# Performance work log

Hardware: AMD Instinct MI355X
Metric: run time of the kernel (lower is better)

The kernel has to match this reference:

```python
import jax, jax.numpy as jnp
import numpy as np

TEMP1, TEMP2, TEMP3 = 4.0, 5.0, 10.0  # forward() default temps
EPS = 1e-8


def setup_inputs() -> dict:
    key = jax.random.key(0)
    k1, k2 = jax.random.split(key)
    B, L, D = 64, 64, 512
    return {
        "ecg_embs": jax.random.normal(k1, (B, L, D), dtype=jnp.float32),
        "sent_embs": jax.random.normal(k2, (B, L, D), dtype=jnp.float32),
    }


def reference(ecg_embs, sent_embs):
    # Fully-batched version of the original per-sample Python loop.
    # i indexes the sentence (query) sample, j the ecg (context) sample.
    B, L, D = ecg_embs.shape
    # scores[i,j,s,q] = <ecg[j,s,:], sent[i,q,:]>  == contextT @ query in torch
    scores = jnp.einsum('jsd,iqd->ijsq', ecg_embs, sent_embs)
    # 1st softmax over query axis q
    attn = jax.nn.softmax(scores, axis=-1)
    # transpose to (i,j,q,s), temperature-scale, 2nd softmax over source axis s
    attn = jax.nn.softmax(TEMP1 * jnp.swapaxes(attn, -1, -2), axis=-1)  # (i,j,q,s)
    # weightedContext[i,j,q,:] = sum_s attn[i,j,q,s] * ecg[j,s,:]
    wctx = jnp.einsum('ijqs,jsd->ijqd', attn, ecg_embs)
    sent = sent_embs[:, None]  # (i,1,q,d) broadcast over j
    w12 = jnp.sum(sent * wctx, axis=-1)
    w1 = jnp.linalg.norm(sent, axis=-1)
    w2 = jnp.linalg.norm(wctx, axis=-1)
    cos = w12 / jnp.maximum(w1 * w2, EPS)  # (i,j,q)
    # row_sim.mul_(temp2).exp_().sum(dim=1).log() ; similarities[j,i] (cat along dim=1)
    sim = TEMP3 * jnp.log(jnp.sum(jnp.exp(TEMP2 * cos), axis=-1)).T  # (j,i)
    labels = jnp.arange(B)
    logp0 = jax.nn.log_softmax(sim, axis=-1)
    logp1 = jax.nn.log_softmax(sim.T, axis=-1)
    loss0 = -jnp.mean(logp0[labels, labels])
    loss1 = -jnp.mean(logp1[labels, labels])
    # att_maps: list of attn[i] from iteration i == diagonal (i==j) attention,
    # each shaped (1, queryL, ih=1, iw=sourceL); stacked -> (B, 1, L, 1, L)
    att_maps = attn[labels, labels][:, None, :, None, :]
    return (loss0 + loss1) / 2.0, att_maps
```

## Files before the change

kernel.cpp:

```cpp
#include <hip/hip_runtime.h>
#include <math.h>

typedef __attribute__((ext_vector_type(8))) short short8;
typedef __attribute__((ext_vector_type(4))) float f32x4;
typedef unsigned int uint;
typedef unsigned short ushort;

#define T1 4.0f
#define T2 5.0f
#define T3 10.0f
#define EPSF 1e-8f
#define SST 68

__device__ inline ushort f2bf(float x) {
    union { float f; uint u; } a; a.f = x;
    uint r = a.u + 0x7FFFu + ((a.u >> 16) & 1u);
    return (ushort)(r >> 16);
}
__device__ inline float bf2f(ushort h) {
    union { uint u; float f; } a; a.u = ((uint)h) << 16;
    return a.f;
}

#define GLDS(gsrc, ldst) \
    __builtin_amdgcn_global_load_lds( \
        (const __attribute__((address_space(1))) uint*)(gsrc), \
        (__attribute__((address_space(3))) uint*)(ldst), 16, 0, 0)

__global__ __launch_bounds__(256) void prep_kernel(
        const float* __restrict__ ecg, const float* __restrict__ sent,
        char* __restrict__ EH, char* __restrict__ EL,
        char* __restrict__ SH, char* __restrict__ SL, float* __restrict__ w1) {
    __shared__ float partial[256];
    const int bid = blockIdx.x;
    const int tensor = bid >> 6, idx = bid & 63;
    const float* src = (tensor ? sent : ecg) + (size_t)idx * 32768;
    char* dh = (tensor ? SH : EH) + (size_t)idx * 65536;
    char* dl = (tensor ? SL : EL) + (size_t)idx * 65536;
    const int tid = threadIdx.x;
    const int r = tid & 63;
    float s2 = 0.f;
    #pragma unroll
    for (int it = 0; it < 4; it++) {
        int kc = it * 4 + (tid >> 6);
        const float* p = src + r * 512 + kc * 32;
        char* oh = dh + kc * 4096 + r * 64;
        char* ol = dl + kc * 4096 + r * 64;
        #pragma unroll
        for (int c = 0; c < 4; c++) {
            float4 v0 = *(const float4*)(p + c * 8);
            float4 v1 = *(const float4*)(p + c * 8 + 4);
            float x[8] = {v0.x, v0.y, v0.z, v0.w, v1.x, v1.y, v1.z, v1.w};
            uint hw[4], lw[4];
            #pragma unroll
            for (int e = 0; e < 4; e++) {
                float a0 = x[2 * e], a1 = x[2 * e + 1];
                ushort h0 = f2bf(a0), h1 = f2bf(a1);
                hw[e] = (uint)h0 | ((uint)h1 << 16);
                ushort l0 = f2bf(a0 - bf2f(h0)), l1 = f2bf(a1 - bf2f(h1));
                lw[e] = (uint)l0 | ((uint)l1 << 16);
                s2 += a0 * a0 + a1 * a1;
            }
            int phys = (c + (r >> 1)) & 3;
            uint4 H; H.x = hw[0]; H.y = hw[1]; H.z = hw[2]; H.w = hw[3];
            *(uint4*)(oh + phys * 16) = H;
            uint4 L; L.x = lw[0]; L.y = lw[1]; L.z = lw[2]; L.w = lw[3];
            *(uint4*)(ol + phys * 16) = L;
        }
    }
    partial[tid] = s2;
    __syncthreads();
    if (tensor == 1 && tid < 64) {
        float t = partial[tid] + partial[tid + 64] + partial[tid + 128] + partial[tid + 192];
        w1[idx * 64 + tid] = sqrtf(t);
    }
}

__global__ __launch_bounds__(256) void gprep_kernel(
        const char* __restrict__ EH, const char* __restrict__ EL, char* __restrict__ Gp) {
    __shared__ __align__(16) char lds[8192];
    const int j = blockIdx.x;
    const int tid = threadIdx.x;
    const int wv = tid >> 6, lane = tid & 63;
    const int wq = wv >> 1, wn = wv & 1;
    const int quad = lane >> 4, ln = lane & 15;
    const char* srcH = EH + (size_t)j * 65536 + wv * 1024 + lane * 16;
    const char* srcL = EL + (size_t)j * 65536 + wv * 1024 + lane * 16;

    int ao[2], bo[2];
    #pragma unroll
    for (int mi = 0; mi < 2; mi++) {
        int R = 32 * wq + 16 * mi + ln;
        ao[mi] = R * 64 + ((quad + (R >> 1)) & 3) * 16;
    }
    #pragma unroll
    for (int ni = 0; ni < 2; ni++) {
        int R = 32 * wn + 16 * ni + ln;
        bo[ni] = R * 64 + ((quad + (R >> 1)) & 3) * 16;
    }

    f32x4 acc[2][2];
    #pragma unroll
    for (int a = 0; a < 2; a++)
        #pragma unroll
        for (int b = 0; b < 2; b++) acc[a][b] = (f32x4){0.f, 0.f, 0.f, 0.f};

    for (int kc = 0; kc < 16; kc++) {
        GLDS(srcH + (size_t)kc * 4096, lds + wv * 1024);
        GLDS(srcL + (size_t)kc * 4096, lds + 4096 + wv * 1024);
        __syncthreads();
        short8 ah[2], al[2], bh[2], bl[2];
        #pragma unroll
        for (int mi = 0; mi < 2; mi++) {
            ah[mi] = *(const short8*)(lds + ao[mi]);
            al[mi] = *(const short8*)(lds + 4096 + ao[mi]);
        }
        #pragma unroll
        for (int ni = 0; ni < 2; ni++) {
            bh[ni] = *(const short8*)(lds + bo[ni]);
            bl[ni] = *(const short8*)(lds + 4096 + bo[ni]);
        }
        #pragma unroll
        for (int mi = 0; mi < 2; mi++)
            #pragma unroll
            for (int ni = 0; ni < 2; ni++) {
                acc[mi][ni] = __builtin_amdgcn_mfma_f32_16x16x32_bf16(ah[mi], bh[ni], acc[mi][ni], 0, 0, 0);
                acc[mi][ni] = __builtin_amdgcn_mfma_f32_16x16x32_bf16(ah[mi], bl[ni], acc[mi][ni], 0, 0, 0);
                acc[mi][ni] = __builtin_amdgcn_mfma_f32_16x16x32_bf16(al[mi], bh[ni], acc[mi][ni], 0, 0, 0);
            }
        __syncthreads();
    }
    #pragma unroll
    for (int mi = 0; mi < 2; mi++)
        #pragma unroll
        for (int ni = 0; ni < 2; ni++)
            #pragma unroll
            for (int r = 0; r < 4; r++) {
                int t = 32 * wq + 16 * mi + quad * 4 + r;
                int u = 32 * wn + 16 * ni + ln;
                float g = acc[mi][ni][r];
                ushort h = f2bf(g);
                ushort l = f2bf(g - bf2f(h));
                char* base = Gp + (size_t)j * 16384 + t * 128 + (((u >> 3) + t) & 7) * 16 + (u & 7) * 2;
                *(ushort*)base = h;
                *(ushort*)(base + 8192) = l;
            }
}

__global__ __launch_bounds__(256, 4) void pair_kernel(
        const char* __restrict__ EH, const char* __restrict__ EL,
        const char* __restrict__ SH, const char* __restrict__ SL,
        const char* __restrict__ Gp, const float* __restrict__ w1g,
        float* __restrict__ simval, float* __restrict__ out) {

    __shared__ __align__(16) char lds[33792];
    __shared__ __align__(16) float mz[64];
    __shared__ float w12all[256], w2all[256];

    const int tid = threadIdx.x;
    const int bn = blockIdx.x;
    const int xcd = bn & 7, slot = bn >> 3;
    const int T = xcd * 8 + (slot >> 4);
    const int wp = slot & 15;
    const int bi = (T >> 3) * 4 + (wp >> 2);
    const int bj = (T & 7) * 4 + (wp & 3);
    const int i0 = bi * 2, j0 = bj * 2;

    const int wv = tid >> 6, lane = tid & 63;
    const int wq = wv >> 1, wn = wv & 1;
    const int quad = lane >> 4, ln = lane & 15;

    int aoff[4], boff[4];
    #pragma unroll
    for (int mi = 0; mi < 4; mi++) {
        int R = 64 * (mi >> 1) + 32 * wq + 16 * (mi & 1) + ln;
        aoff[mi] = R * 64 + ((quad + (R >> 1)) & 3) * 16;
    }
    #pragma unroll
    for (int ni = 0; ni < 4; ni++) {
        int R = 64 * (ni >> 1) + 32 * wn + 16 * (ni & 1) + ln;
        boff[ni] = 16384 + R * 64 + ((quad + (R >> 1)) & 3) * 16;
    }

    const char* gA; const char* gB; int ldoff;
    if (wv == 0)      { gA = EH + (size_t)j0 * 65536;       gB = EH + (size_t)(j0 + 1) * 65536; ldoff = 0; }
    else if (wv == 1) { gA = EL + (size_t)j0 * 65536;       gB = EL + (size_t)(j0 + 1) * 65536; ldoff = 8192; }
    else if (wv == 2) { gA = SH + (size_t)i0 * 65536;       gB = SH + (size_t)(i0 + 1) * 65536; ldoff = 16384; }
    else              { gA = SL + (size_t)i0 * 65536;       gB = SL + (size_t)(i0 + 1) * 65536; ldoff = 24576; }
    gA += lane * 16; gB += lane * 16;

    f32x4 acc[4][4];
    #pragma unroll
    for (int a = 0; a < 4; a++)
        #pragma unroll
        for (int b = 0; b < 4; b++) acc[a][b] = (f32x4){0.f, 0.f, 0.f, 0.f};

    for (int kc = 0; kc < 16; kc++) {
        #pragma unroll
        for (int n = 0; n < 4; n++) GLDS(gA + n * 1024, lds + ldoff + n * 1024);
        #pragma unroll
        for (int n = 0; n < 4; n++) GLDS(gB + n * 1024, lds + ldoff + 4096 + n * 1024);
        gA += 4096; gB += 4096;
        __syncthreads();
        short8 bh[4], bl[4];
        #pragma unroll
        for (int ni = 0; ni < 4; ni++) {
            bh[ni] = *(const short8*)(lds + boff[ni]);
            bl[ni] = *(const short8*)(lds + boff[ni] + 8192);
        }
        #pragma unroll
        for (int mi = 0; mi < 4; mi++) {
            short8 ah = *(const short8*)(lds + aoff[mi]);
            short8 al = *(const short8*)(lds + aoff[mi] + 8192);
            #pragma unroll
            for (int ni = 0; ni < 4; ni++) {
                acc[mi][ni] = __builtin_amdgcn_mfma_f32_16x16x32_bf16(ah, bh[ni], acc[mi][ni], 0, 0, 0);
                acc[mi][ni] = __builtin_amdgcn_mfma_f32_16x16x32_bf16(ah, bl[ni], acc[mi][ni], 0, 0, 0);
                acc[mi][ni] = __builtin_amdgcn_mfma_f32_16x16x32_bf16(al, bh[ni], acc[mi][ni], 0, 0, 0);
            }
        }
        __syncthreads();
    }

    float* SsT = (float*)lds;
    float* yT  = (float*)lds;
    char*  Pb  = lds + 17408;

    #pragma unroll
    for (int pr = 0; pr < 4; pr++) {
        const int a = pr >> 1, b = pr & 1;
        const int i = i0 + b, j = j0 + a;

        #pragma unroll
        for (int dm = 0; dm < 2; dm++)
            #pragma unroll
            for (int dn = 0; dn < 2; dn++) {
                int s0 = 32 * wq + 16 * dm + quad * 4;
                int q  = 32 * wn + 16 * dn + ln;
                *(f32x4*)(SsT + q * SST + s0) = acc[2 * a + dm][2 * b + dn];
            }
        __syncthreads();

        {
            const int s = tid >> 2, c = tid & 3;
            float vv[16]; float m = -1e30f;
            #pragma unroll
            for (int t = 0; t < 16; t++) {
                int tt = (t + 4 * c) & 15;
                vv[t] = SsT[(16 * c + tt) * SST + s];
                m = fmaxf(m, vv[t]);
            }
            m = fmaxf(m, __shfl_xor(m, 1));
            m = fmaxf(m, __shfl_xor(m, 2));
            float sum = 0.f;
            #pragma unroll
            for (int t = 0; t < 16; t++) sum += __expf(vv[t] - m);
            sum += __shfl_xor(sum, 1);
            sum += __shfl_xor(sum, 2);
            if (c == 0) mz[s] = m + __logf(sum);
        }
        __syncthreads();

        {
            const int q = tid >> 2, c = tid & 3;
            float sc[16], at[16];
            #pragma unroll
            for (int r4 = 0; r4 < 4; r4++)
                *(f32x4*)(sc + 4 * r4) = *(const f32x4*)(SsT + q * SST + 16 * c + 4 * r4);
            float mzv[16];
            #pragma unroll
            for (int r4 = 0; r4 < 4; r4++)
                *(f32x4*)(mzv + 4 * r4) = *(const f32x4*)(mz + 16 * c + 4 * r4);
            float m2 = -1e30f;
            #pragma unroll
            for (int t = 0; t < 16; t++) {
                at[t] = __expf(sc[t] - mzv[t]);
                m2 = fmaxf(m2, T1 * at[t]);
            }
            m2 = fmaxf(m2, __shfl_xor(m2, 1));
            m2 = fmaxf(m2, __shfl_xor(m2, 2));
            float sum = 0.f;
            #pragma unroll
            for (int t = 0; t < 16; t++) { at[t] = __expf(T1 * at[t] - m2); sum += at[t]; }
            sum += __shfl_xor(sum, 1);
            sum += __shfl_xor(sum, 2);
            float inv = 1.f / sum;
            float p12 = 0.f;
            #pragma unroll
            for (int t = 0; t < 16; t++) { at[t] *= inv; p12 += at[t] * sc[t]; }
            p12 += __shfl_xor(p12, 1);
            p12 += __shfl_xor(p12, 2);
            if (c == 0) w12all[pr * 64 + q] = p12;

            if (i == j) {
                float* om = out + 1 + (size_t)i * 4096;
                #pragma unroll
                for (int t = 0; t < 16; t++) om[q * 64 + c * 16 + t] = at[t];
            }

            uint hw[8], lw[8];
            #pragma unroll
            for (int e = 0; e < 8; e++) {
                ushort h0 = f2bf(at[2 * e]), h1 = f2bf(at[2 * e + 1]);
                hw[e] = (uint)h0 | ((uint)h1 << 16);
                ushort l0 = f2bf(at[2 * e] - bf2f(h0)), l1 = f2bf(at[2 * e + 1] - bf2f(h1));
                lw[e] = (uint)l0 | ((uint)l1 << 16);
            }
            int p0 = (2 * c + q) & 7, p1 = (2 * c + 1 + q) & 7;
            uint4 W;
            W.x = hw[0]; W.y = hw[1]; W.z = hw[2]; W.w = hw[3];
            *(uint4*)(Pb + q * 128 + p0 * 16) = W;
            W.x = hw[4]; W.y = hw[5]; W.z = hw[6]; W.w = hw[7];
            *(uint4*)(Pb + q * 128 + p1 * 16) = W;
            W.x = lw[0]; W.y = lw[1]; W.z = lw[2]; W.w = lw[3];
            *(uint4*)(Pb + 8192 + q * 128 + p0 * 16) = W;
            W.x = lw[4]; W.y = lw[5]; W.z = lw[6]; W.w = lw[7];
            *(uint4*)(Pb + 8192 + q * 128 + p1 * 16) = W;
        }
        __syncthreads();

        {
            const char* gs = Gp + (size_t)j * 16384 + wv * 4096 + lane * 16;
            char* gd = lds + wv * 4096;
            GLDS(gs,        gd);
            GLDS(gs + 1024, gd + 1024);
            GLDS(gs + 2048, gd + 2048);
            GLDS(gs + 3072, gd + 3072);
        }
        __syncthreads();

        f32x4 acc2[2][2];
        #pragma unroll
        for (int x = 0; x < 2; x++)
            #pragma unroll
            for (int y = 0; y < 2; y++) acc2[x][y] = (f32x4){0.f, 0.f, 0.f, 0.f};
        #pragma unroll
        for (int ch = 0; ch < 2; ch++) {
            short8 pah[2], pal[2], gbh[2], gbl[2];
            #pragma unroll
            for (int m2i = 0; m2i < 2; m2i++) {
                int q = 32 * wq + 16 * m2i + ln;
                int ph = ((ch * 4 + quad) + q) & 7;
                pah[m2i] = *(const short8*)(Pb + q * 128 + ph * 16);
                pal[m2i] = *(const short8*)(Pb + 8192 + q * 128 + ph * 16);
            }
            #pragma unroll
            for (int n2i = 0; n2i < 2; n2i++) {
                int u = 32 * wn + 16 * n2i + ln;
                int ph = ((ch * 4 + quad) + u) & 7;
                gbh[n2i] = *(const short8*)(lds + u * 128 + ph * 16);
                gbl[n2i] = *(const short8*)(lds + 8192 + u * 128 + ph * 16);
            }
            #pragma unroll
            for (int m2i = 0; m2i < 2; m2i++)
                #pragma unroll
                for (int n2i = 0; n2i < 2; n2i++) {
                    acc2[m2i][n2i] = __builtin_amdgcn_mfma_f32_16x16x32_bf16(pah[m2i], gbh[n2i], acc2[m2i][n2i], 0, 0, 0);
                    acc2[m2i][n2i] = __builtin_amdgcn_mfma_f32_16x16x32_bf16(pah[m2i], gbl[n2i], acc2[m2i][n2i], 0, 0, 0);
                    acc2[m2i][n2i] = __builtin_amdgcn_mfma_f32_16x16x32_bf16(pal[m2i], gbh[n2i], acc2[m2i][n2i], 0, 0, 0);
                }
        }
        __syncthreads();

        #pragma unroll
        for (int m2i = 0; m2i < 2; m2i++)
            #pragma unroll
            for (int n2i = 0; n2i < 2; n2i++) {
                int q0 = 32 * wq + 16 * m2i + quad * 4;
                int t  = 32 * wn + 16 * n2i + ln;
                *(f32x4*)(yT + t * SST + q0) = acc2[m2i][n2i];
            }
        __syncthreads();

        {
            const int q = tid >> 2, c = tid & 3;
            int p0 = (2 * c + q) & 7, p1 = (2 * c + 1 + q) & 7;
            uint4 H0 = *(const uint4*)(Pb + q * 128 + p0 * 16);
            uint4 H1 = *(const uint4*)(Pb + q * 128 + p1 * 16);
            uint4 L0 = *(const uint4*)(Pb + 8192 + q * 128 + p0 * 16);
            uint4 L1 = *(const uint4*)(Pb + 8192 + q * 128 + p1 * 16);
            uint hw[8] = {H0.x,H0.y,H0.z,H0.w, H1.x,H1.y,H1.z,H1.w};
            uint lw[8] = {L0.x,L0.y,L0.z,L0.w, L1.x,L1.y,L1.z,L1.w};
            float s = 0.f;
            #pragma unroll
            for (int e = 0; e < 8; e++) {
                float q0v = bf2f((ushort)(hw[e] & 0xFFFFu)) + bf2f((ushort)(lw[e] & 0xFFFFu));
                float q1v = bf2f((ushort)(hw[e] >> 16))     + bf2f((ushort)(lw[e] >> 16));
                s += q0v * yT[(16 * c + 2 * e) * SST + q];
                s += q1v * yT[(16 * c + 2 * e + 1) * SST + q];
            }
            s += __shfl_xor(s, 1);
            s += __shfl_xor(s, 2);
            if (c == 0) w2all[pr * 64 + q] = s;
        }
        __syncthreads();
    }

    {
        const int pr = wv;
        const int ii = i0 + (pr & 1), jj = j0 + (pr >> 1);
        float w2 = sqrtf(fmaxf(w2all[pr * 64 + lane], 0.f));
        float cosv = w12all[pr * 64 + lane] / fmaxf(w1g[ii * 64 + lane] * w2, EPSF);
        float e = __expf(T2 * cosv);
        #pragma unroll
        for (int off = 32; off; off >>= 1) e += __shfl_down(e, off);
        if (lane == 0) simval[ii * 64 + jj] = T3 * __logf(e);
    }
}

__global__ __launch_bounds__(256) void loss_kernel(const float* __restrict__ val,
                                                   float* __restrict__ out) {
    __shared__ float v[4096];
    const int tid = threadIdx.x;
    #pragma unroll
    for (int k = 0; k < 4; k++)
        ((float4*)v)[tid + k * 256] = ((const float4*)val)[tid + k * 256];
    __syncthreads();
    if (tid < 64) {
        int i = tid;
        float rmax = -1e30f, cmax = -1e30f;
        for (int jj = 0; jj < 64; jj++) {
            rmax = fmaxf(rmax, v[i * 64 + jj]);
            cmax = fmaxf(cmax, v[jj * 64 + i]);
        }
        float rs = 0.f, cs = 0.f;
        for (int jj = 0; jj < 64; jj++) {
            rs += __expf(v[i * 64 + jj] - rmax);
            cs += __expf(v[jj * 64 + i] - cmax);
        }
        float rlse = rmax + __logf(rs);
        float clse = cmax + __logf(cs);
        float part = 2.f * v[i * 64 + i] - rlse - clse;
        #pragma unroll
        for (int off = 32; off; off >>= 1) part += __shfl_down(part, off);
        if (i == 0) out[0] = -part / 128.f;
    }
}

extern "C" void kernel_launch(void* const* d_in, const int* in_sizes, int n_in,
                              void* d_out, int out_size, void* d_ws, size_t ws_size,
                              hipStream_t stream) {
    (void)in_sizes; (void)n_in; (void)out_size; (void)ws_size;
    const float* ecg  = (const float*)d_in[0];
    const float* sent = (const float*)d_in[1];
    float* out = (float*)d_out;

    char* ws = (char*)d_ws;
    float* w1v  = (float*)ws;
    float* simv = (float*)(ws + 16384);
    char* EH = ws + 32768;
    char* EL = EH + (size_t)64 * 65536;
    char* SH = EL + (size_t)64 * 65536;
    char* SL = SH + (size_t)64 * 65536;
    char* Gp = SL + (size_t)64 * 65536;

    prep_kernel <<<128, 256, 0, stream>>>(ecg, sent, EH, EL, SH, SL, w1v);
    gprep_kernel<<<64,  256, 0, stream>>>(EH, EL, Gp);
    pair_kernel <<<1024, 256, 0, stream>>>(EH, EL, SH, SL, Gp, w1v, simv, out);
    loss_kernel <<<1,   256, 0, stream>>>(simv, out);
}
```

Baseline: 150.4 us.

## Double-buffer pair kernel K loop, split gprep into more blocks, parallelize loss reductions

The pair kernel's K-loop now double-buffers LDS (64KB). It prefetches the next chunk while computing the current one, using vmcnt waits and raw barriers, and lowers the launch-bound occupancy hint from 4 to 2. gprep is split into 4x more blocks, each computing one 16-row tile with direct global loads and no LDS staging. The loss kernel computes row and column log-sum-exps on separate wavefronts. The aim is to hide global load latency and add parallelism, at the cost of fewer resident blocks per CU in the pair kernel.

```diff
diff --git a/kernel.cpp b/kernel.cpp
--- a/kernel.cpp
+++ b/kernel.cpp
@@ -78,82 +78,52 @@
 
 __global__ __launch_bounds__(256) void gprep_kernel(
         const char* __restrict__ EH, const char* __restrict__ EL, char* __restrict__ Gp) {
-    __shared__ __align__(16) char lds[8192];
-    const int j = blockIdx.x;
+    const int b = blockIdx.x;
+    const int j = b >> 2, tq = b & 3;
     const int tid = threadIdx.x;
     const int wv = tid >> 6, lane = tid & 63;
-    const int wq = wv >> 1, wn = wv & 1;
     const int quad = lane >> 4, ln = lane & 15;
-    const char* srcH = EH + (size_t)j * 65536 + wv * 1024 + lane * 16;
-    const char* srcL = EL + (size_t)j * 65536 + wv * 1024 + lane * 16;
-
-    int ao[2], bo[2];
-    #pragma unroll
-    for (int mi = 0; mi < 2; mi++) {
-        int R = 32 * wq + 16 * mi + ln;
-        ao[mi] = R * 64 + ((quad + (R >> 1)) & 3) * 16;
-    }
-    #pragma unroll
-    for (int ni = 0; ni < 2; ni++) {
-        int R = 32 * wn + 16 * ni + ln;
-        bo[ni] = R * 64 + ((quad + (R >> 1)) & 3) * 16;
-    }
-
-    f32x4 acc[2][2];
-    #pragma unroll
-    for (int a = 0; a < 2; a++)
-        #pragma unroll
-        for (int b = 0; b < 2; b++) acc[a][b] = (f32x4){0.f, 0.f, 0.f, 0.f};
-
+    const char* srcH = EH + (size_t)j * 65536;
+    const char* srcL = EL + (size_t)j * 65536;
+
+    const int Ra = 16 * tq + ln;
+    const int ao = Ra * 64 + ((quad + (Ra >> 1)) & 3) * 16;
+    const int Rb = 16 * wv + ln;
+    const int bo = Rb * 64 + ((quad + (Rb >> 1)) & 3) * 16;
+
+    f32x4 acc = (f32x4){0.f, 0.f, 0.f, 0.f};
+    #pragma unroll 4
     for (int kc = 0; kc < 16; kc++) {
-        GLDS(srcH + (size_t)kc * 4096, lds + wv * 1024);
-        GLDS(srcL + (size_t)kc * 4096, lds + 4096 + wv * 1024);
-        __syncthreads();
-        short8 ah[2], al[2], bh[2], bl[2];
-        #pragma unroll
-        for (int mi = 0; mi < 2; mi++) {
-            ah[mi] = *(const short8*)(lds + ao[mi]);
-            al[mi] = *(const short8*)(lds + 4096 + ao[mi]);
-        }
-        #pragma unroll
-        for (int ni = 0; ni < 2; ni++) {
-            bh[ni] = *(const short8*)(lds + bo[ni]);
-            bl[ni] = *(const short8*)(lds + 4096 + bo[ni]);
-        }
-        #pragma unroll
-        for (int mi = 0; mi < 2; mi++)
-            #pragma unroll
-            for (int ni = 0; ni < 2; ni++) {
-                acc[mi][ni] = __builtin_amdgcn_mfma_f32_16x16x32_bf16(ah[mi], bh[ni], acc[mi][ni], 0, 0, 0);
-                acc[mi][ni] = __builtin_amdgcn_mfma_f32_16x16x32_bf16(ah[mi], bl[ni], acc[mi][ni], 0, 0, 0);
-                acc[mi][ni] = __builtin_amdgcn_mfma_f32_16x16x32_bf16(al[mi], bh[ni], acc[mi][ni], 0, 0, 0);
-            }
-        __syncthreads();
-    }
-    #pragma unroll
-    for (int mi = 0; mi < 2; mi++)
-        #pragma unroll
-        for (int ni = 0; ni < 2; ni++)
-            #pragma unroll
-            for (int r = 0; r < 4; r++) {
-                int t = 32 * wq + 16 * mi + quad * 4 + r;
-                int u = 32 * wn + 16 * ni + ln;
-                float g = acc[mi][ni][r];
-                ushort h = f2bf(g);
-                ushort l = f2bf(g - bf2f(h));
-                char* base = Gp + (size_t)j * 16384 + t * 128 + (((u >> 3) + t) & 7) * 16 + (u & 7) * 2;
-                *(ushort*)base = h;
-                *(ushort*)(base + 8192) = l;
-            }
-}
-
-__global__ __launch_bounds__(256, 4) void pair_kernel(
+        const char* ph = srcH + (size_t)kc * 4096;
+        const char* pl = srcL + (size_t)kc * 4096;
+        short8 ah = *(const short8*)(ph + ao);
+        short8 al = *(const short8*)(pl + ao);
+        short8 bh = *(const short8*)(ph + bo);
+        short8 bl = *(const short8*)(pl + bo);
+        acc = __builtin_amdgcn_mfma_f32_16x16x32_bf16(ah, bh, acc, 0, 0, 0);
+        acc = __builtin_amdgcn_mfma_f32_16x16x32_bf16(ah, bl, acc, 0, 0, 0);
+        acc = __builtin_amdgcn_mfma_f32_16x16x32_bf16(al, bh, acc, 0, 0, 0);
+    }
+    #pragma unroll
+    for (int rr = 0; rr < 4; rr++) {
+        int t = 16 * tq + quad * 4 + rr;
+        int u = 16 * wv + ln;
+        float g = acc[rr];
+        ushort h = f2bf(g);
+        ushort l = f2bf(g - bf2f(h));
+        char* base = Gp + (size_t)j * 16384 + t * 128 + (((u >> 3) + t) & 7) * 16 + (u & 7) * 2;
+        *(ushort*)base = h;
+        *(ushort*)(base + 8192) = l;
+    }
+}
+
+__global__ __launch_bounds__(256, 2) void pair_kernel(
         const char* __restrict__ EH, const char* __restrict__ EL,
         const char* __restrict__ SH, const char* __restrict__ SL,
         const char* __restrict__ Gp, const float* __restrict__ w1g,
         float* __restrict__ simval, float* __restrict__ out) {
 
-    __shared__ __align__(16) char lds[33792];
+    __shared__ __align__(16) char lds[65536];
     __shared__ __align__(16) float mz[64];
     __shared__ float w12all[256], w2all[256];
 
@@ -195,23 +165,17 @@
         #pragma unroll
         for (int b = 0; b < 4; b++) acc[a][b] = (f32x4){0.f, 0.f, 0.f, 0.f};
 
-    for (int kc = 0; kc < 16; kc++) {
-        #pragma unroll
-        for (int n = 0; n < 4; n++) GLDS(gA + n * 1024, lds + ldoff + n * 1024);
-        #pragma unroll
-        for (int n = 0; n < 4; n++) GLDS(gB + n * 1024, lds + ldoff + 4096 + n * 1024);
-        gA += 4096; gB += 4096;
-        __syncthreads();
+    auto compute = [&](const char* L) {
         short8 bh[4], bl[4];
         #pragma unroll
         for (int ni = 0; ni < 4; ni++) {
-            bh[ni] = *(const short8*)(lds + boff[ni]);
-            bl[ni] = *(const short8*)(lds + boff[ni] + 8192);
+            bh[ni] = *(const short8*)(L + boff[ni]);
+            bl[ni] = *(const short8*)(L + boff[ni] + 8192);
         }
         #pragma unroll
         for (int mi = 0; mi < 4; mi++) {
-            short8 ah = *(const short8*)(lds + aoff[mi]);
-            short8 al = *(const short8*)(lds + aoff[mi] + 8192);
+            short8 ah = *(const short8*)(L + aoff[mi]);
+            short8 al = *(const short8*)(L + aoff[mi] + 8192);
             #pragma unroll
             for (int ni = 0; ni < 4; ni++) {
                 acc[mi][ni] = __builtin_amdgcn_mfma_f32_16x16x32_bf16(ah, bh[ni], acc[mi][ni], 0, 0, 0);
@@ -219,8 +183,35 @@
                 acc[mi][ni] = __builtin_amdgcn_mfma_f32_16x16x32_bf16(al, bh[ni], acc[mi][ni], 0, 0, 0);
             }
         }
-        __syncthreads();
-    }
+    };
+
+    #pragma unroll
+    for (int n = 0; n < 4; n++) GLDS(gA + n * 1024, lds + ldoff + n * 1024);
+    #pragma unroll
+    for (int n = 0; n < 4; n++) GLDS(gB + n * 1024, lds + ldoff + 4096 + n * 1024);
+
+    for (int kc = 0; kc < 15; kc++) {
+        {
+            const char* pA = gA + (size_t)(kc + 1) * 4096;
+            const char* pB = gB + (size_t)(kc + 1) * 4096;
+            char* db = lds + ((kc + 1) & 1) * 32768 + ldoff;
+            #pragma unroll
+            for (int n = 0; n < 4; n++) GLDS(pA + n * 1024, db + n * 1024);
+            #pragma unroll
+            for (int n = 0; n < 4; n++) GLDS(pB + n * 1024, db + 4096 + n * 1024);
+        }
+        asm volatile("s_waitcnt vmcnt(8)" ::: "memory");
+        __builtin_amdgcn_s_barrier();
+        asm volatile("" ::: "memory");
+        compute(lds + (kc & 1) * 32768);
+        asm volatile("" ::: "memory");
+        __builtin_amdgcn_s_barrier();
+    }
+    asm volatile("s_waitcnt vmcnt(0)" ::: "memory");
+    __builtin_amdgcn_s_barrier();
+    asm volatile("" ::: "memory");
+    compute(lds + 32768);
+    __syncthreads();
 
     float* SsT = (float*)lds;
     float* yT  = (float*)lds;
@@ -411,6 +402,7 @@
 __global__ __launch_bounds__(256) void loss_kernel(const float* __restrict__ val,
                                                    float* __restrict__ out) {
     __shared__ float v[4096];
+    __shared__ float rlse[64], clse[64];
     const int tid = threadIdx.x;
     #pragma unroll
     for (int k = 0; k < 4; k++)
@@ -418,22 +410,25 @@
     __syncthreads();
     if (tid < 64) {
         int i = tid;
-        float rmax = -1e30f, cmax = -1e30f;
-        for (int jj = 0; jj < 64; jj++) {
-            rmax = fmaxf(rmax, v[i * 64 + jj]);
-            cmax = fmaxf(cmax, v[jj * 64 + i]);
-        }
-        float rs = 0.f, cs = 0.f;
-        for (int jj = 0; jj < 64; jj++) {
-            rs += __expf(v[i * 64 + jj] - rmax);
-            cs += __expf(v[jj * 64 + i] - cmax);
-        }
-        float rlse = rmax + __logf(rs);
-        float clse = cmax + __logf(cs);
-        float part = 2.f * v[i * 64 + i] - rlse - clse;
+        float rmax = -1e30f;
+        for (int jj = 0; jj < 64; jj++) rmax = fmaxf(rmax, v[i * 64 + jj]);
+        float rs = 0.f;
+        for (int jj = 0; jj < 64; jj++) rs += __expf(v[i * 64 + jj] - rmax);
+        rlse[i] = rmax + __logf(rs);
+    } else if (tid < 128) {
+        int i = tid - 64;
+        float cmax = -1e30f;
+        for (int jj = 0; jj < 64; jj++) cmax = fmaxf(cmax, v[jj * 64 + i]);
+        float cs = 0.f;
+        for (int jj = 0; jj < 64; jj++) cs += __expf(v[jj * 64 + i] - cmax);
+        clse[i] = cmax + __logf(cs);
+    }
+    __syncthreads();
+    if (tid < 64) {
+        float part = 2.f * v[tid * 64 + tid] - rlse[tid] - clse[tid];
         #pragma unroll
         for (int off = 32; off; off >>= 1) part += __shfl_down(part, off);
-        if (i == 0) out[0] = -part / 128.f;
+        if (tid == 0) out[0] = -part / 128.f;
     }
 }
 
@@ -455,7 +450,7 @@
     char* Gp = SL + (size_t)64 * 65536;
 
     prep_kernel <<<128, 256, 0, stream>>>(ecg, sent, EH, EL, SH, SL, w1v);
-    gprep_kernel<<<64,  256, 0, stream>>>(EH, EL, Gp);
+    gprep_kernel<<<256, 256, 0, stream>>>(EH, EL, Gp);
     pair_kernel <<<1024, 256, 0, stream>>>(EH, EL, SH, SL, Gp, w1v, simv, out);
     loss_kernel <<<1,   256, 0, stream>>>(simv, out);
 }
```

Measured after the change: 152.4 us. No clear change (+1.3%).
